# Performance work log

Hardware: AMD Instinct MI355X
Metric: run time of the kernel (lower is better)

## Reference

```python
import jax, jax.numpy as jnp
import numpy as np

BS, SL, NC = 512, 1024, 64


def setup_inputs() -> dict:
    key = jax.random.key(0)
    k1, k2, k3, k4 = jax.random.split(key, 4)
    inputs = jax.random.normal(k1, (BS, SL, NC), dtype=jnp.float32)
    # valid-suffix padding masks: True = padded position (as in the torch module)
    lengths = jax.random.randint(k2, (BS,), SL // 2, SL + 1)
    masks = jnp.arange(SL)[None, :] >= lengths[:, None]  # bool [BS, SL]
    tag_indices = jax.random.randint(k3, (BS, SL), 0, NC).astype(jnp.int64)
    transitions = jax.random.normal(k4, (NC, NC), dtype=jnp.float32) * 0.01
    return {"inputs": inputs, "masks": masks, "tag_indices": tag_indices,
            "transitions": transitions}


def _crf_loss(inputs, masks, tag_indices, transitions):
    bs, sl, nc = inputs.shape
    # unary score: emission at gold tag per step, padded steps zeroed
    unary = jnp.take_along_axis(inputs, tag_indices[..., None], axis=2)[..., 0]
    unary = jnp.where(masks, 0.0, unary).sum(axis=1)  # [bs]
    # binary score: transition between consecutive gold tags
    binary = transitions[tag_indices[:, :-1], tag_indices[:, 1:]]  # [bs, sl-1]
    binary = jnp.where(masks[:, 1:], 0.0, binary).sum(axis=1)  # [bs]
    # log partition via forward algorithm (lax.scan over time)
    def step(alphas, xs):
        x_t, m_t = xs  # [bs, nc], [bs]
        scores = alphas[:, :, None] + transitions[None, :, :]  # [bs, nc(from), nc(to)]
        new_alphas = x_t + jax.nn.logsumexp(scores, axis=1)
        alphas = jnp.where(m_t[:, None], alphas, new_alphas)
        return alphas, None

    xs = (jnp.swapaxes(inputs[:, 1:, :], 0, 1), jnp.swapaxes(masks[:, 1:], 0, 1))
    alphas, _ = jax.lax.scan(step, inputs[:, 0, :], xs)
    log_norm = jax.nn.logsumexp(alphas, axis=1)  # [bs]
    log_likelihood = unary + binary - log_norm
    loss = jnp.sum(-log_likelihood) / bs  # batch_average=True
    return loss


def reference(inputs, masks, tag_indices, transitions):
    loss = _crf_loss(inputs, masks, tag_indices, transitions)
    return (loss, transitions)
```

## Files before the change

### kernel.cpp

```cpp
#include <hip/hip_runtime.h>

#define BS 512
#define SL 1024
#define NC 64

template <int CTRL>
__device__ __forceinline__ float dppf(float x) {
    return __int_as_float(__builtin_amdgcn_mov_dpp(__float_as_int(x), CTRL, 0xF, 0xF, true));
}
__device__ __forceinline__ float rflf(float x) {
    return __int_as_float(__builtin_amdgcn_readfirstlane(__float_as_int(x)));
}

__device__ __forceinline__ void halfswap32(float x, float& r0, float& r1) {
#if __has_builtin(__builtin_amdgcn_permlane32_swap)
    auto r = __builtin_amdgcn_permlane32_swap(__float_as_int(x), __float_as_int(x), false, false);
    r0 = __int_as_float(r[0]); r1 = __int_as_float(r[1]);
#else
    float w = __shfl_xor(x, 32, 64);
    bool up = (threadIdx.x & 32) != 0;
    r0 = up ? w : x;
    r1 = up ? x : w;
#endif
}
__device__ __forceinline__ void halfswap16(float x, float& r0, float& r1) {
#if __has_builtin(__builtin_amdgcn_permlane16_swap)
    auto r = __builtin_amdgcn_permlane16_swap(__float_as_int(x), __float_as_int(x), false, false);
    r0 = __int_as_float(r[0]); r1 = __int_as_float(r[1]);
#else
    float w = __int_as_float(__builtin_amdgcn_ds_swizzle(__float_as_int(x), 0x401F));
    bool up = (threadIdx.x & 16) != 0;
    r0 = up ? w : x;
    r1 = up ? x : w;
#endif
}

__device__ __forceinline__ float wave_sum(float x) {
    x += dppf<0xB1>(x);
    x += dppf<0x4E>(x);
    x += dppf<0x141>(x);
    x += dppf<0x140>(x);
    float a, c;
    halfswap16(x, a, c); x = a + c;
    halfswap32(x, a, c); x = a + c;
    return x;
}

__global__ __launch_bounds__(256) void crf_init_out(const float* __restrict__ trans,
                                                    float* __restrict__ out) {
    int idx = blockIdx.x * 256 + threadIdx.x;
    if (idx == 0) out[0] = 0.0f;
    if (idx < NC * NC) out[1 + idx] = trans[idx];
}

__global__ __launch_bounds__(256) void crf_ub(const float* __restrict__ inputs,
                                              const int* __restrict__ masks,
                                              const int* __restrict__ tags,
                                              const float* __restrict__ trans,
                                              float* __restrict__ out) {
    const int b = blockIdx.x;
    const int tid = threadIdx.x;
    const int* tg = tags + (size_t)b * SL;
    const int* mk = masks + (size_t)b * SL;
    const float* xb = inputs + (size_t)b * SL * NC;

    float acc = 0.0f;
    const int t0 = tid * 4;
    int tprev = (t0 > 0) ? tg[t0 - 1] : 0;
#pragma unroll
    for (int j = 0; j < 4; ++j) {
        int t = t0 + j;
        int tgt = tg[t];
        if (mk[t] == 0) {
            acc += xb[(size_t)t * NC + tgt];
            if (t > 0) acc += trans[tprev * NC + tgt];
        }
        tprev = tgt;
    }

    acc = wave_sum(acc);
    __shared__ float r[4];
    if ((tid & 63) == 0) r[tid >> 6] = acc;
    __syncthreads();
    if (tid == 0) atomicAdd(out, -(r[0] + r[1] + r[2] + r[3]) * (1.0f / BS));
}

__global__ __launch_bounds__(64) __attribute__((amdgpu_waves_per_eu(1)))
void crf_fwd(const float* __restrict__ inputs,
             const int* __restrict__ masks,
             const float* __restrict__ trans,
             float* __restrict__ out) {
    const int b = blockIdx.x;
    const int lane = threadIdx.x;
    const float* __restrict__ xp = inputs + (size_t)b * SL * NC;

    int len = 0;
#pragma unroll
    for (int k = 0; k < SL / NC; ++k) {
        unsigned long long bal = __ballot(masks[(size_t)b * SL + k * NC + lane] == 0);
        len += __popcll(bal);
    }

    int B[4];
    {
        float pf = __int_as_float(lane);
        float p0, p1, a0, a1, c0, c1;
        halfswap32(pf, p0, p1);
        halfswap16(p0, a0, a1);
        halfswap16(p1, c0, c1);
        B[0] = __builtin_amdgcn_readfirstlane(__float_as_int(a0));
        B[1] = __builtin_amdgcn_readfirstlane(__float_as_int(a1));
        B[2] = __builtin_amdgcn_readfirstlane(__float_as_int(c0));
        B[3] = __builtin_amdgcn_readfirstlane(__float_as_int(c1));
    }

    float E[64];
#pragma unroll
    for (int f = 0; f < 4; ++f) {
#pragma unroll
        for (int m = 0; m < 16; ++m) {
            int row = B[f] + ((lane ^ m) & 15);
            E[f * 16 + m] = __expf(trans[row * NC + lane]);
        }
    }
#pragma unroll
    for (int i = 0; i < 64; ++i) {
        asm volatile("" : "+v"(E[i]));
    }

    float x0 = xp[lane];
    float base = rflf(x0);
    float q = __expf(x0 - base);

    float ex  = __expf(xp[NC + lane]);
    float xn1 = xp[2 * NC + lane];
    float xn2 = xp[3 * NC + lane];

    for (int t = 1; t < len; ++t) {
        int t3 = t + 3; if (t3 > SL - 1) t3 = SL - 1;
        float xnew = xp[(size_t)t3 * NC + lane];
        float exn = __expf(xn1);

        float m  = rflf(q);
        float rm = __builtin_amdgcn_rcpf(m);
        float ex_eff = ex * rm;
        base += __logf(m);

        float h0, h1, h2, h3, u0, u1;
        halfswap32(q, u0, u1);
        halfswap16(u0, h0, h1);
        halfswap16(u1, h2, h3);
        float a0 = 0.f, a1 = 0.f, a2 = 0.f, a3 = 0.f;
        float a4 = 0.f, a5 = 0.f, a6 = 0.f, a7 = 0.f;
#pragma unroll
        for (int f = 0; f < 4; ++f) {
            float v0 = (f == 0) ? h0 : (f == 1) ? h1 : (f == 2) ? h2 : h3;
            float v1  = dppf<0xB1>(v0);
            float v2  = dppf<0x4E>(v0);
            float v3  = dppf<0x4E>(v1);
            float v7  = dppf<0x141>(v0);
            float v6  = dppf<0x141>(v1);
            float v5  = dppf<0x141>(v2);
            float v4  = dppf<0x141>(v3);
            a0 = fmaf(v0, E[f * 16 + 0], a0);
            a1 = fmaf(v1, E[f * 16 + 1], a1);
            a2 = fmaf(v2, E[f * 16 + 2], a2);
            a3 = fmaf(v3, E[f * 16 + 3], a3);
            float v15 = dppf<0x140>(v0);
            float v14 = dppf<0x140>(v1);
            float v13 = dppf<0x140>(v2);
            float v12 = dppf<0x140>(v3);
            a4 = fmaf(v4, E[f * 16 + 4], a4);
            a5 = fmaf(v5, E[f * 16 + 5], a5);
            a6 = fmaf(v6, E[f * 16 + 6], a6);
            a7 = fmaf(v7, E[f * 16 + 7], a7);
            float v11 = dppf<0x140>(v4);
            float v10 = dppf<0x140>(v5);
            float v9  = dppf<0x140>(v6);
            float v8  = dppf<0x140>(v7);
            a0 = fmaf(v8,  E[f * 16 + 8],  a0);
            a1 = fmaf(v9,  E[f * 16 + 9],  a1);
            a2 = fmaf(v10, E[f * 16 + 10], a2);
            a3 = fmaf(v11, E[f * 16 + 11], a3);
            a4 = fmaf(v12, E[f * 16 + 12], a4);
            a5 = fmaf(v13, E[f * 16 + 13], a5);
            a6 = fmaf(v14, E[f * 16 + 14], a6);
            a7 = fmaf(v15, E[f * 16 + 15], a7);
        }
        float s = ((a0 + a1) + (a2 + a3)) + ((a4 + a5) + (a6 + a7));
        q = s * ex_eff;

        ex = exn; xn1 = xn2; xn2 = xnew;
    }

    float qsum = wave_sum(q);
    float log_norm = base + __logf(qsum);
    if (lane == 0) atomicAdd(out, log_norm * (1.0f / BS));
}

extern "C" void kernel_launch(void* const* d_in, const int* in_sizes, int n_in,
                              void* d_out, int out_size, void* d_ws, size_t ws_size,
                              hipStream_t stream) {
    const float* inputs = (const float*)d_in[0];
    const int*   masks  = (const int*)d_in[1];
    const int*   tags   = (const int*)d_in[2];
    const float* trans  = (const float*)d_in[3];
    float* out = (float*)d_out;

    crf_init_out<<<(1 + NC * NC + 255) / 256, 256, 0, stream>>>(trans, out);
    crf_ub<<<BS, 256, 0, stream>>>(inputs, masks, tags, trans, out);
    crf_fwd<<<BS, 64, 0, stream>>>(inputs, masks, trans, out);
}
```

Measured before the change: 597.7 us.

## Move transition matrix and alpha broadcast from registers/DPP into swizzled LDS

```diff
diff --git a/kernel.cpp b/kernel.cpp
--- a/kernel.cpp
+++ b/kernel.cpp
@@ -11,7 +11,6 @@
 __device__ __forceinline__ float rflf(float x) {
     return __int_as_float(__builtin_amdgcn_readfirstlane(__float_as_int(x)));
 }
-
 __device__ __forceinline__ void halfswap32(float x, float& r0, float& r1) {
 #if __has_builtin(__builtin_amdgcn_permlane32_swap)
     auto r = __builtin_amdgcn_permlane32_swap(__float_as_int(x), __float_as_int(x), false, false);
@@ -19,8 +18,7 @@
 #else
     float w = __shfl_xor(x, 32, 64);
     bool up = (threadIdx.x & 32) != 0;
-    r0 = up ? w : x;
-    r1 = up ? x : w;
+    r0 = up ? w : x; r1 = up ? x : w;
 #endif
 }
 __device__ __forceinline__ void halfswap16(float x, float& r0, float& r1) {
@@ -30,11 +28,9 @@
 #else
     float w = __int_as_float(__builtin_amdgcn_ds_swizzle(__float_as_int(x), 0x401F));
     bool up = (threadIdx.x & 16) != 0;
-    r0 = up ? w : x;
-    r1 = up ? x : w;
+    r0 = up ? w : x; r1 = up ? x : w;
 #endif
 }
-
 __device__ __forceinline__ float wave_sum(float x) {
     x += dppf<0xB1>(x);
     x += dppf<0x4E>(x);
@@ -77,7 +73,6 @@
         }
         tprev = tgt;
     }
-
     acc = wave_sum(acc);
     __shared__ float r[4];
     if ((tid & 63) == 0) r[tid >> 6] = acc;
@@ -85,14 +80,17 @@
     if (tid == 0) atomicAdd(out, -(r[0] + r[1] + r[2] + r[3]) * (1.0f / BS));
 }
 
-__global__ __launch_bounds__(64) __attribute__((amdgpu_waves_per_eu(1)))
+__global__ __launch_bounds__(64)
 void crf_fwd(const float* __restrict__ inputs,
              const int* __restrict__ masks,
              const float* __restrict__ trans,
              float* __restrict__ out) {
     const int b = blockIdx.x;
     const int lane = threadIdx.x;
+    const int k7 = lane & 7;
     const float* __restrict__ xp = inputs + (size_t)b * SL * NC;
+
+    __shared__ float lds[64 * 64 + 8 * 68];
 
     int len = 0;
 #pragma unroll
@@ -101,32 +99,25 @@
         len += __popcll(bal);
     }
 
-    int B[4];
-    {
-        float pf = __int_as_float(lane);
-        float p0, p1, a0, a1, c0, c1;
-        halfswap32(pf, p0, p1);
-        halfswap16(p0, a0, a1);
-        halfswap16(p1, c0, c1);
-        B[0] = __builtin_amdgcn_readfirstlane(__float_as_int(a0));
-        B[1] = __builtin_amdgcn_readfirstlane(__float_as_int(a1));
-        B[2] = __builtin_amdgcn_readfirstlane(__float_as_int(c0));
-        B[3] = __builtin_amdgcn_readfirstlane(__float_as_int(c1));
+#pragma unroll
+    for (int G = 0; G < 16; ++G) {
+        int pos = G ^ k7;
+#pragma unroll
+        for (int e = 0; e < 4; ++e)
+            lds[64 * lane + 4 * pos + e] = __expf(trans[(4 * G + e) * NC + lane]);
     }
 
-    float E[64];
+    int qaddr[8];
+    {
+        int g = lane >> 2, e = lane & 3;
 #pragma unroll
-    for (int f = 0; f < 4; ++f) {
-#pragma unroll
-        for (int m = 0; m < 16; ++m) {
-            int row = B[f] + ((lane ^ m) & 15);
-            E[f * 16 + m] = __expf(trans[row * NC + lane]);
-        }
+        for (int k = 0; k < 8; ++k)
+            qaddr[k] = 64 * 64 + 68 * k + 4 * (g ^ k) + e;
     }
-#pragma unroll
-    for (int i = 0; i < 64; ++i) {
-        asm volatile("" : "+v"(E[i]));
-    }
+    const float* Erow = &lds[64 * lane];
+    const float* Qrow = &lds[64 * 64 + 68 * k7];
+
+    __syncthreads();
 
     float x0 = xp[lane];
     float base = rflf(x0);
@@ -146,48 +137,28 @@
         float ex_eff = ex * rm;
         base += __logf(m);
 
-        float h0, h1, h2, h3, u0, u1;
-        halfswap32(q, u0, u1);
-        halfswap16(u0, h0, h1);
-        halfswap16(u1, h2, h3);
+#pragma unroll
+        for (int k = 0; k < 8; ++k) lds[qaddr[k]] = q;
+
         float a0 = 0.f, a1 = 0.f, a2 = 0.f, a3 = 0.f;
         float a4 = 0.f, a5 = 0.f, a6 = 0.f, a7 = 0.f;
 #pragma unroll
-        for (int f = 0; f < 4; ++f) {
-            float v0 = (f == 0) ? h0 : (f == 1) ? h1 : (f == 2) ? h2 : h3;
-            float v1  = dppf<0xB1>(v0);
-            float v2  = dppf<0x4E>(v0);
-            float v3  = dppf<0x4E>(v1);
-            float v7  = dppf<0x141>(v0);
-            float v6  = dppf<0x141>(v1);
-            float v5  = dppf<0x141>(v2);
-            float v4  = dppf<0x141>(v3);
-            a0 = fmaf(v0, E[f * 16 + 0], a0);
-            a1 = fmaf(v1, E[f * 16 + 1], a1);
-            a2 = fmaf(v2, E[f * 16 + 2], a2);
-            a3 = fmaf(v3, E[f * 16 + 3], a3);
-            float v15 = dppf<0x140>(v0);
-            float v14 = dppf<0x140>(v1);
-            float v13 = dppf<0x140>(v2);
-            float v12 = dppf<0x140>(v3);
-            a4 = fmaf(v4, E[f * 16 + 4], a4);
-            a5 = fmaf(v5, E[f * 16 + 5], a5);
-            a6 = fmaf(v6, E[f * 16 + 6], a6);
-            a7 = fmaf(v7, E[f * 16 + 7], a7);
-            float v11 = dppf<0x140>(v4);
-            float v10 = dppf<0x140>(v5);
-            float v9  = dppf<0x140>(v6);
-            float v8  = dppf<0x140>(v7);
-            a0 = fmaf(v8,  E[f * 16 + 8],  a0);
-            a1 = fmaf(v9,  E[f * 16 + 9],  a1);
-            a2 = fmaf(v10, E[f * 16 + 10], a2);
-            a3 = fmaf(v11, E[f * 16 + 11], a3);
-            a4 = fmaf(v12, E[f * 16 + 12], a4);
-            a5 = fmaf(v13, E[f * 16 + 13], a5);
-            a6 = fmaf(v14, E[f * 16 + 14], a6);
-            a7 = fmaf(v15, E[f * 16 + 15], a7);
+        for (int j = 0; j < 16; j += 2) {
+            float4 ev0 = *(const float4*)(Erow + 4 * j);
+            float4 qv0 = *(const float4*)(Qrow + 4 * j);
+            float4 ev1 = *(const float4*)(Erow + 4 * (j + 1));
+            float4 qv1 = *(const float4*)(Qrow + 4 * (j + 1));
+            a0 = fmaf(qv0.x, ev0.x, a0);
+            a1 = fmaf(qv0.y, ev0.y, a1);
+            a2 = fmaf(qv0.z, ev0.z, a2);
+            a3 = fmaf(qv0.w, ev0.w, a3);
+            a4 = fmaf(qv1.x, ev1.x, a4);
+            a5 = fmaf(qv1.y, ev1.y, a5);
+            a6 = fmaf(qv1.z, ev1.z, a6);
+            a7 = fmaf(qv1.w, ev1.w, a7);
         }
         float s = ((a0 + a1) + (a2 + a3)) + ((a4 + a5) + (a6 + a7));
+
         q = s * ex_eff;
 
         ex = exn; xn1 = xn2; xn2 = xnew;
```

Measured after the change: 1.140 ms. 90.7% more time.
